# Performance work log

Measured on AMD Instinct MI355X. Metric: run time of the kernel, lower is better.

Reference implementation:

```python
import jax, jax.numpy as jnp
import numpy as np
from jax.scipy.special import logsumexp

UNK_ID = 1
B, T, V = 128, 33, 25000
E, H, D = 256, 256, 512
N, C = 8192, 16384
L = T - 1


def setup_inputs() -> dict:
    key = jax.random.key(0)
    ks = jax.random.split(key, 12)
    input_memories = jax.random.normal(ks[0], (N, D), jnp.float32)
    # each target owns a contiguous block of N//B memories (every segment non-empty)
    origin = jnp.repeat(jnp.arange(B, dtype=jnp.int32), N // B)
    initial_states = jax.random.normal(ks[1], (B, H), jnp.float32)
    target_token_ids = jax.random.randint(ks[2], (B, T), 0, V)
    # copyable elements: pick (memory n, time l); flat idx into [N,L] and [B,L]
    mem_pick = jax.random.randint(ks[3], (C,), 0, N)
    t_pick = jax.random.randint(ks[4], (C,), 0, L)
    copyable_elements_idxs = mem_pick * L + t_pick
    copyable_elements_sample_idxs = origin[mem_pick] * L + t_pick
    target_lengths = jax.random.randint(ks[5], (B,), 1, L + 1)
    emb_weight = 0.02 * jax.random.normal(ks[6], (V, E), jnp.float32)
    gru_w_ih = 0.05 * jax.random.normal(ks[7], (3 * H, E), jnp.float32)
    gru_w_hh = 0.05 * jax.random.normal(ks[8], (3 * H, H), jnp.float32)
    gru_b_ih = jnp.zeros((3 * H,), jnp.float32)
    gru_b_hh = jnp.zeros((3 * H,), jnp.float32)
    w_std_att = 0.05 * jax.random.normal(ks[9], (H, D), jnp.float32)
    w_copy_att = 0.05 * jax.random.normal(ks[10], (H, D), jnp.float32)
    hidden_to_vocab = 0.01 * jax.random.normal(ks[11], (2 * H, E), jnp.float32)
    vocab_bias = jnp.zeros((V,), jnp.float32)
    return dict(input_memories=input_memories, input_memories_origin_idx=origin,
                initial_states=initial_states, target_token_ids=target_token_ids,
                copyable_elements_idxs=copyable_elements_idxs,
                copyable_elements_sample_idxs=copyable_elements_sample_idxs,
                target_lengths=target_lengths, emb_weight=emb_weight,
                gru_w_ih=gru_w_ih, gru_w_hh=gru_w_hh, gru_b_ih=gru_b_ih,
                gru_b_hh=gru_b_hh, w_std_att=w_std_att, w_copy_att=w_copy_att,
                hidden_to_vocab=hidden_to_vocab, vocab_bias=vocab_bias)


def _gru(x, h0, w_ih, w_hh, b_ih, b_hh):
    # x: [B,L,E], h0: [B,H] -> outputs [B,L,H], last state [B,H]
    def step(h, xt):
        gi = xt @ w_ih.T + b_ih
        gh = h @ w_hh.T + b_hh
        ir, iz, inew = jnp.split(gi, 3, axis=-1)
        hr, hz, hnew = jnp.split(gh, 3, axis=-1)
        r = jax.nn.sigmoid(ir + hr)
        z = jax.nn.sigmoid(iz + hz)
        n = jnp.tanh(inew + r * hnew)
        h_next = (1.0 - z) * n + z * h
        return h_next, h_next
    h_last, ys = jax.lax.scan(step, h0, jnp.swapaxes(x, 0, 1))
    return jnp.swapaxes(ys, 0, 1), h_last


def _seg_log_softmax(x, idx, num_seg):
    m = jax.ops.segment_max(x, idx, num_segments=num_seg)
    x_sh = x - m[idx]
    s = jax.ops.segment_sum(jnp.exp(x_sh), idx, num_segments=num_seg)
    return x_sh - jnp.log(s)[idx]


def _seg_logsumexp(x, idx, num_seg):
    m = jax.ops.segment_max(x, idx, num_segments=num_seg)
    m_safe = jnp.where(jnp.isfinite(m), m, 0.0)
    s = jax.ops.segment_sum(jnp.exp(x - m_safe[idx]), idx, num_segments=num_seg)
    return jnp.where(s > 0, jnp.log(jnp.where(s > 0, s, 1.0)) + m_safe, -jnp.inf)


def reference(input_memories, input_memories_origin_idx, initial_states,
              target_token_ids, copyable_elements_idxs,
              copyable_elements_sample_idxs, target_lengths, emb_weight,
              gru_w_ih, gru_w_hh, gru_b_ih, gru_b_hh, w_std_att, w_copy_att,
              hidden_to_vocab, vocab_bias):
    origin = input_memories_origin_idx
    b, t = target_token_ids.shape
    l = t - 1
    tok_in = target_token_ids[:, :-1]
    tok_out = target_token_ids[:, 1:]

    x = emb_weight[tok_in]                                   # [B,L,E]
    out_states, _ = _gru(x, initial_states, gru_w_ih, gru_w_hh, gru_b_ih, gru_b_hh)
    std_reps = input_memories @ w_std_att.T                  # [N,H]
    copy_reps = input_memories @ w_copy_att.T                # [N,H]
    out_per_input = out_states[origin]                       # [N,L,H]
    std_scores = jnp.einsum('nlh,nh->nl', out_per_input, std_reps)
    copy_scores = jnp.einsum('nlh,nh->nl', out_per_input, copy_reps)

    std_logprobs = _seg_log_softmax(std_scores, origin, b)   # [N,L]
    std_mul = jnp.exp(std_logprobs)[:, :, None] * std_reps[:, None, :]
    std_out = jax.ops.segment_sum(std_mul, origin, num_segments=b)  # [B,L,H]

    cat = jnp.concatenate([std_out, out_states], axis=-1)    # [B,L,2H]
    target_scores = (cat @ hidden_to_vocab) @ emb_weight.T + vocab_bias  # [B,L,V]

    total_copy = _seg_logsumexp(copy_scores, origin, b)      # [B,L]
    all_scores = jnp.concatenate([target_scores, total_copy[:, :, None]], axis=-1)
    norm = logsumexp(all_scores, axis=-1)                    # [B,L]
    target_logprobs = target_scores - norm[:, :, None]
    copy_logprobs = copy_scores - norm[origin]               # [N,L]

    num_valid = jax.ops.segment_sum(jnp.ones_like(copyable_elements_sample_idxs),
                                    copyable_elements_sample_idxs,
                                    num_segments=b * l)
    valid_copy = num_valid.reshape(b, l) > 0
    unk_loc = tok_out == UNK_ID
    mask = valid_copy & unk_loc

    gen_lp = jnp.take_along_axis(target_logprobs, tok_out[:, :, None], axis=-1)[..., 0]
    gen_lp = jnp.where(mask, -jnp.inf, gen_lp)

    cc = _seg_logsumexp(copy_logprobs.reshape(-1)[copyable_elements_idxs],
                        copyable_elements_sample_idxs, b * l).reshape(b, l)

    any_lp = logsumexp(jnp.stack([gen_lp, cc]), axis=0)      # [B,L]
    len_mask = (jnp.arange(l)[None, :] < target_lengths[:, None]).astype(jnp.float32)
    per_seq = (any_lp * len_mask).sum(-1) / len_mask.sum(-1)
    return -per_seq.mean()
```

## Files before the change

kernel.cpp:

```cpp
#include <hip/hip_runtime.h>
#include <hip/hip_bf16.h>

#define UNK 1
constexpr int B  = 128, T = 33, V = 25000, E = 256, H = 256, D = 512;
constexpr int N  = 8192, C = 16384, L = 32;
constexpr int BL = B * L;
constexpr int VP = 25088;

typedef __attribute__((ext_vector_type(8))) short bf16x8;
typedef __attribute__((ext_vector_type(4))) float fx4;
typedef unsigned short u16;
typedef unsigned int u32;

__device__ __forceinline__ u16 f2b(float f) {
  u32 u = __float_as_uint(f);
  u += 0x7FFFu + ((u >> 16) & 1u);
  return (u16)(u >> 16);
}
__device__ __forceinline__ float b2f(u16 s) { return __uint_as_float(((u32)s) << 16); }
__device__ __forceinline__ float fsigm(float x) { return 1.f / (1.f + __expf(-x)); }
__device__ __forceinline__ float ftanh(float x) {
  float cx = fminf(fmaxf(x, -15.f), 15.f);
  float e = __expf(2.f * cx);
  return (e - 1.f) / (e + 1.f);
}
__device__ __forceinline__ u32 fkey(float f) {
  u32 b = __float_as_uint(f);
  return (b & 0x80000000u) ? ~b : (b | 0x80000000u);
}
__device__ __forceinline__ float fdec(u32 k) {
  u32 b = (k & 0x80000000u) ? (k & 0x7FFFFFFFu) : ~k;
  return __uint_as_float(b);
}
__device__ __forceinline__ void lcomb(float& M, float& S, float m2, float s2) {
  float Mn = fmaxf(M, m2);
  float a = (S  > 0.f) ? S  * expf(M  - Mn) : 0.f;
  float b = (s2 > 0.f) ? s2 * expf(m2 - Mn) : 0.f;
  M = Mn; S = a + b;
}
__device__ __forceinline__ void gload16(const void* g, void* l) {
  __builtin_amdgcn_global_load_lds(
      (const __attribute__((address_space(1))) void*)g,
      (__attribute__((address_space(3))) void*)l, 16, 0, 0);
}

__device__ __forceinline__ void cvt4_at(const float* in, u16* out, int i) {
  float4 v = *(const float4*)&in[i];
  u16 r[4] = { f2b(v.x), f2b(v.y), f2b(v.z), f2b(v.w) };
  *(ushort4*)&out[i] = *(ushort4*)r;
}

constexpr int EB_GI   = 192;
constexpr int P2_MEM  = N * D / 1024;
constexpr int P2_WHH  = 192;
constexpr int P2_WS   = 128;
constexpr int P2_WC   = 128;
constexpr int EB2_TOT = EB_GI + P2_MEM + P2_WHH + P2_WS + P2_WC;

__global__ __launch_bounds__(256, 2) void k_embgiB2(const int* __restrict__ tok,
    const float* __restrict__ emb, const float* __restrict__ wih,
    const float* __restrict__ bih, const float* __restrict__ bhh,
    float* __restrict__ Git,
    const float* __restrict__ mem, const float* __restrict__ whh,
    const float* __restrict__ wstd, const float* __restrict__ wcpy,
    u16* __restrict__ memb, u16* __restrict__ whb,
    u16* __restrict__ wsb, u16* __restrict__ wcb) {
  __shared__ __align__(16) u16 As[2][128 * 64];
  __shared__ __align__(16) u16 Bs2[2][128 * 64];
  int e = blockIdx.x, t = threadIdx.x;
  if (e >= EB_GI) {
    int b = e - EB_GI;
    if (b < P2_MEM) { cvt4_at(mem, memb, (b * 256 + t) * 4); return; }
    b -= P2_MEM;
    if (b < P2_WHH) { cvt4_at(whh, whb, (b * 256 + t) * 4); return; }
    b -= P2_WHH;
    if (b < P2_WS)  { cvt4_at(wstd, wsb, (b * 256 + t) * 4); return; }
    b -= P2_WS;
    cvt4_at(wcpy, wcb, (b * 256 + t) * 4);
    return;
  }
  int m0 = (e & 31) * 128, n0 = (e >> 5) * 128;
  int lane = t & 63, w = t >> 6, wm = w >> 1, wn = w & 1;
  int r16 = lane & 15, hi = lane >> 4;
  char* AsB = (char*)&As[0][0];
  char* BsB = (char*)&Bs2[0][0];
  int tk4[4];
#pragma unroll
  for (int i = 0; i < 4; ++i) {
    int row = (w * 4 + i) * 8 + (lane >> 3);
    int bl = m0 + row;
    tk4[i] = tok[(bl >> 5) * 33 + (bl & 31)];
  }
  fx4 acc[4][4] = {};
  auto stage = [&](int kt, int buf) {
#pragma unroll
    for (int i = 0; i < 4; ++i) {
      int row = (w * 4 + i) * 8 + (lane >> 3);
      int c = (lane & 7) ^ (row & 7);
      float4 a0 = *(const float4*)&emb[tk4[i] * 256 + kt * 64 + c * 8];
      float4 a1 = *(const float4*)&emb[tk4[i] * 256 + kt * 64 + c * 8 + 4];
      __align__(16) u16 ra[8] = { f2b(a0.x), f2b(a0.y), f2b(a0.z), f2b(a0.w),
                                  f2b(a1.x), f2b(a1.y), f2b(a1.z), f2b(a1.w) };
      *(int4*)(AsB + buf * 16384 + (w * 4 + i) * 1024 + lane * 16) = *(const int4*)ra;
      float4 b0 = *(const float4*)&wih[(n0 + row) * 256 + kt * 64 + c * 8];
      float4 b1 = *(const float4*)&wih[(n0 + row) * 256 + kt * 64 + c * 8 + 4];
      __align__(16) u16 rb[8] = { f2b(b0.x), f2b(b0.y), f2b(b0.z), f2b(b0.w),
                                  f2b(b1.x), f2b(b1.y), f2b(b1.z), f2b(b1.w) };
      *(int4*)(BsB + buf * 16384 + (w * 4 + i) * 1024 + lane * 16) = *(const int4*)rb;
    }
  };
  stage(0, 0);
  __syncthreads();
  for (int kt = 0; kt < 4; ++kt) {
    int buf = kt & 1;
    bf16x8 afr[4][2], bfr[4][2];
#pragma unroll
    for (int mi = 0; mi < 4; ++mi)
#pragma unroll
      for (int kk = 0; kk < 2; ++kk) {
        int row = wm * 64 + mi * 16 + r16, cc = kk * 4 + hi;
        afr[mi][kk] = *(const bf16x8*)(AsB + buf * 16384 + (row * 8 + (cc ^ (row & 7))) * 16);
      }
#pragma unroll
    for (int ni = 0; ni < 4; ++ni)
#pragma unroll
      for (int kk = 0; kk < 2; ++kk) {
        int row = wn * 64 + ni * 16 + r16, cc = kk * 4 + hi;
        bfr[ni][kk] = *(const bf16x8*)(BsB + buf * 16384 + (row * 8 + (cc ^ (row & 7))) * 16);
      }
    if (kt < 3) {
      stage(kt + 1, (kt + 1) & 1);
    }
#pragma unroll
    for (int kk = 0; kk < 2; ++kk)
#pragma unroll
      for (int mi = 0; mi < 4; ++mi)
#pragma unroll
        for (int ni = 0; ni < 4; ++ni)
          acc[mi][ni] = __builtin_amdgcn_mfma_f32_16x16x32_bf16(afr[mi][kk], bfr[ni][kk], acc[mi][ni], 0, 0, 0);
    __syncthreads();
  }
  float bihv[4];
#pragma unroll
  for (int ni = 0; ni < 4; ++ni) {
    int j = n0 + wn * 64 + ni * 16 + r16;
    bihv[ni] = bih[j] + (j < 512 ? bhh[j] : 0.f);
  }
#pragma unroll
  for (int mi = 0; mi < 4; ++mi)
#pragma unroll
    for (int ni = 0; ni < 4; ++ni)
#pragma unroll
      for (int q = 0; q < 4; ++q) {
        int bl = m0 + wm * 64 + mi * 16 + hi * 4 + q;
        int b = bl >> 5, st = bl & 31;
        int j  = n0 + wn * 64 + ni * 16 + r16;
        Git[(((size_t)(b >> 4) * 32 + st) * 768 + j) * 16 + (b & 15)] = acc[mi][ni][q] + bihv[ni];
      }
}

constexpr int GR_GRU  = 8;
constexpr int GR_REPS = 128;
constexpr int GR_EMB  = VP * E / 2048;
constexpr int GR_TR   = 256;
constexpr int GR_INIT = 8;
constexpr int GR_TOT  = GR_GRU + GR_REPS + GR_EMB + GR_TR + GR_INIT;

__global__ __launch_bounds__(512, 2) void k_grureps(
    const float* __restrict__ Git, const u16* __restrict__ whb,
    const float* __restrict__ bhh, const float* __restrict__ h0,
    u16* __restrict__ outsb,
    const u16* __restrict__ Am, const u16* __restrict__ wsb,
    const u16* __restrict__ wcb, float* __restrict__ sr, float* __restrict__ cr,
    const float* __restrict__ emb, const float* __restrict__ h2v,
    u16* __restrict__ embb, u16* __restrict__ h2vtb,
    u32* __restrict__ segk, float* __restrict__ segs,
    int* __restrict__ nval, float* __restrict__ lacc) {
  __shared__ __align__(16) char smem[147456];
  const int t = threadIdx.x;
  const int w = t >> 6, l = t & 63;

  if (blockIdx.x >= GR_GRU + GR_REPS) {
    int b = blockIdx.x - (GR_GRU + GR_REPS);
    if (b < GR_EMB) {
      int i = (b * 512 + t) * 4;
      if (i + 3 < V * E) cvt4_at(emb, embb, i);
      else for (int j = 0; j < 4; ++j) embb[i + j] = (i + j < V * E) ? f2b(emb[i + j]) : (u16)0;
      return;
    }
    b -= GR_EMB;
    if (b < GR_TR) {
      int f = b * 512 + t, j = f >> 9, k = f & 511;
      h2vtb[f] = f2b(h2v[k * 256 + j]);
      return;
    }
    b -= GR_TR;
    int i = b * 512 + t;
    if (i < BL) { segk[i] = 0x007FFFFFu; segs[i] = 0.f; nval[i] = 0; }
    if (i == 0) lacc[0] = 0.f;
    return;
  }

  if (blockIdx.x < GR_GRU) {
    u16* nfr = (u16*)smem;
    u16* hbf0 = (u16*)(smem + 131072);
    u16* hbf1 = (u16*)(smem + 131072 + 8192);
    const int lj = l & 15, lk = l >> 4;
    const int b0 = blockIdx.x * 16;

    bf16x8 fr[2][8], fz[2][8];
#pragma unroll
    for (int jh = 0; jh < 2; ++jh)
#pragma unroll
      for (int kc = 0; kc < 8; ++kc) {
        int jr = w * 32 + jh * 16 + lj;
        int k0 = kc * 32 + lk * 8;
        fr[jh][kc] = *(const bf16x8*)&whb[(0 * 256 + jr) * 256 + k0];
        fz[jh][kc] = *(const bf16x8*)&whb[(1 * 256 + jr) * 256 + k0];
        int4 nv = *(const int4*)&whb[(2 * 256 + jr) * 256 + k0];
        *(int4*)&nfr[((w * 16 + jh * 8 + kc) * 64 + l) * 8] = nv;
      }
    float bN[2];
#pragma unroll
    for (int jh = 0; jh < 2; ++jh) bN[jh] = bhh[512 + w * 32 + jh * 16 + lj];
    float hst[2][4];
#pragma unroll
    for (int jh = 0; jh < 2; ++jh)
#pragma unroll
      for (int q = 0; q < 4; ++q) {
        int m = lk * 4 + q, j = w * 32 + jh * 16 + lj;
        hst[jh][q] = h0[(b0 + m) * 256 + j];
        hbf0[m * 256 + (((j >> 3) ^ (m & 7)) * 8) + (j & 7)] = f2b(hst[jh][q]);
      }
    __syncthreads();

    for (int st = 0; st < 32; ++st) {
      const float* gb = Git + (size_t)(blockIdx.x * 32 + st) * 768 * 16;
      fx4 grz[4];
#pragma unroll
      for (int g = 0; g < 2; ++g)
#pragma unroll
        for (int jh = 0; jh < 2; ++jh)
          grz[g * 2 + jh] = *(const fx4*)&gb[(g * 256 + w * 32 + jh * 16 + lj) * 16 + lk * 4];
      fx4 gn[2];
      fx4 accR[2] = {}, accZ[2] = {}, accN[2] = {};
      const u16* hb = (st & 1) ? hbf1 : hbf0;
#pragma unroll
      for (int kc = 0; kc < 8; ++kc) {
        int k8 = kc * 4 + lk;
        bf16x8 a = *(const bf16x8*)&hb[lj * 256 + ((k8 ^ (lj & 7)) * 8)];
        bf16x8 nf0 = *(const bf16x8*)&nfr[((w * 16 + 0 + kc) * 64 + l) * 8];
        bf16x8 nf1 = *(const bf16x8*)&nfr[((w * 16 + 8 + kc) * 64 + l) * 8];
        accR[0] = __builtin_amdgcn_mfma_f32_16x16x32_bf16(a, fr[0][kc], accR[0], 0, 0, 0);
        accR[1] = __builtin_amdgcn_mfma_f32_16x16x32_bf16(a, fr[1][kc], accR[1], 0, 0, 0);
        accZ[0] = __builtin_amdgcn_mfma_f32_16x16x32_bf16(a, fz[0][kc], accZ[0], 0, 0, 0);
        accZ[1] = __builtin_amdgcn_mfma_f32_16x16x32_bf16(a, fz[1][kc], accZ[1], 0, 0, 0);
        accN[0] = __builtin_amdgcn_mfma_f32_16x16x32_bf16(a, nf0, accN[0], 0, 0, 0);
        accN[1] = __builtin_amdgcn_mfma_f32_16x16x32_bf16(a, nf1, accN[1], 0, 0, 0);
        if (kc == 5) {
#pragma unroll
          for (int jh = 0; jh < 2; ++jh)
            gn[jh] = *(const fx4*)&gb[(2 * 256 + w * 32 + jh * 16 + lj) * 16 + lk * 4];
        }
      }
      u16* hw = (st & 1) ? hbf0 : hbf1;
#pragma unroll
      for (int jh = 0; jh < 2; ++jh)
#pragma unroll
        for (int q = 0; q < 4; ++q) {
          float r = fsigm(grz[jh][q] + accR[jh][q]);
          float z = fsigm(grz[2 + jh][q] + accZ[jh][q]);
          float n = ftanh(gn[jh][q] + r * (accN[jh][q] + bN[jh]));
          float hn = (1.f - z) * n + z * hst[jh][q];
          hst[jh][q] = hn;
          int m = lk * 4 + q, j = w * 32 + jh * 16 + lj;
          u16 hbv = f2b(hn);
          hw[m * 256 + (((j >> 3) ^ (m & 7)) * 8) + (j & 7)] = hbv;
          outsb[((size_t)(b0 + m) * 32 + st) * 256 + j] = hbv;
        }
      __syncthreads();
    }
    return;
  }

  int rb = blockIdx.x - GR_GRU;
  int m0 = (rb >> 1) * 128, sn = rb & 1;
  const u16* Bsrc = sn ? wcb : wsb;
  int grp = w >> 2, wg = w & 3, wm = wg >> 1, wn = wg & 1;
  int jb = grp * 128;
  int lane = l, r16 = lane & 15, hi = lane >> 4;
  char* AsB = smem;
  char* BsB = smem + 32768 + grp * 32768;
  fx4 acc[4][4] = {};
  auto stage = [&](int kt, int buf) {
    if (grp == 0) {
#pragma unroll
      for (int i = 0; i < 4; ++i) {
        int s = (wg * 4 + i) * 64 + lane;
        int row = s >> 3, sw = s & 7, c = sw ^ (row & 7);
        gload16(&Am[(m0 + row) * 512 + kt * 64 + c * 8], AsB + buf * 16384 + (wg * 4 + i) * 1024);
        gload16(&Bsrc[(0 + row) * 512 + kt * 64 + c * 8], (smem + 32768) + buf * 16384 + (wg * 4 + i) * 1024);
      }
    } else {
#pragma unroll
      for (int i = 0; i < 4; ++i) {
        int s = (wg * 4 + i) * 64 + lane;
        int row = s >> 3, sw = s & 7, c = sw ^ (row & 7);
        gload16(&Bsrc[(128 + row) * 512 + kt * 64 + c * 8], (smem + 65536) + buf * 16384 + (wg * 4 + i) * 1024);
      }
    }
  };
  stage(0, 0);
  for (int kt = 0; kt < 8; ++kt) {
    __syncthreads();
    if (kt < 7) stage(kt + 1, (kt + 1) & 1);
    int buf = kt & 1;
    bf16x8 afr[4][2], bfr[4][2];
#pragma unroll
    for (int mi = 0; mi < 4; ++mi)
#pragma unroll
      for (int kk = 0; kk < 2; ++kk) {
        int row = wm * 64 + mi * 16 + r16, cc = kk * 4 + hi;
        afr[mi][kk] = *(const bf16x8*)(AsB + buf * 16384 + (row * 8 + (cc ^ (row & 7))) * 16);
      }
#pragma unroll
    for (int ni = 0; ni < 4; ++ni)
#pragma unroll
      for (int kk = 0; kk < 2; ++kk) {
        int row = wn * 64 + ni * 16 + r16, cc = kk * 4 + hi;
        bfr[ni][kk] = *(const bf16x8*)(BsB + buf * 16384 + (row * 8 + (cc ^ (row & 7))) * 16);
      }
#pragma unroll
    for (int kk = 0; kk < 2; ++kk)
#pragma unroll
      for (int mi = 0; mi < 4; ++mi)
#pragma unroll
        for (int ni = 0; ni < 4; ++ni)
          acc[mi][ni] = __builtin_amdgcn_mfma_f32_16x16x32_bf16(afr[mi][kk], bfr[ni][kk], acc[mi][ni], 0, 0, 0);
  }
#pragma unroll
  for (int mi = 0; mi < 4; ++mi)
#pragma unroll
    for (int ni = 0; ni < 4; ++ni)
#pragma unroll
      for (int q = 0; q < 4; ++q) {
        int mr = m0 + wm * 64 + mi * 16 + hi * 4 + q;
        int j  = sn * 256 + jb + wn * 64 + ni * 16 + r16;
        float vv = acc[mi][ni][q];
        if (j < 256) sr[mr * 256 + j] = vv; else cr[mr * 256 + (j - 256)] = vv;
      }
}

__global__ void k_scores(const u16* __restrict__ outsb, const float* __restrict__ sr,
                         const float* __restrict__ cr, float* __restrict__ ss,
                         float* __restrict__ cs) {
  __shared__ float os[32][257];
  int b = blockIdx.x >> 2, nc = blockIdx.x & 3, t = threadIdx.x;
  for (int i = 0; i < 8; ++i) {
    int q = t + 256 * i, row = q >> 6, c4 = q & 63;
    ushort4 v = *(const ushort4*)&outsb[(b * 32 + row) * 256 + c4 * 4];
    os[row][c4 * 4] = b2f(v.x); os[row][c4 * 4 + 1] = b2f(v.y);
    os[row][c4 * 4 + 2] = b2f(v.z); os[row][c4 * 4 + 3] = b2f(v.w);
  }
  __syncthreads();
  int l = t & 31, g = t >> 5;
  for (int rep = 0; rep < 2; ++rep) {
    int n = b * 64 + nc * 16 + g + rep * 8;
    float a = 0.f, c = 0.f;
    for (int k4 = 0; k4 < 64; ++k4) {
      float4 s4 = *(const float4*)&sr[n * 256 + k4 * 4];
      float4 c4v = *(const float4*)&cr[n * 256 + k4 * 4];
      float o0 = os[l][k4 * 4], o1 = os[l][k4 * 4 + 1];
      float o2 = os[l][k4 * 4 + 2], o3 = os[l][k4 * 4 + 3];
      a = fmaf(o0, s4.x, a); a = fmaf(o1, s4.y, a);
      a = fmaf(o2, s4.z, a); a = fmaf(o3, s4.w, a);
      c = fmaf(o0, c4v.x, c); c = fmaf(o1, c4v.y, c);
      c = fmaf(o2, c4v.z, c); c = fmaf(o3, c4v.w, c);
    }
    ss[n * 32 + l] = a; cs[n * 32 + l] = c;
  }
}

__global__ void k_smxseg(const float* __restrict__ ss, const float* __restrict__ cs,
                         const float* __restrict__ sr, u16* __restrict__ sob,
                         float* __restrict__ tc,
                         const int* __restrict__ idx, const int* __restrict__ sid,
                         u32* __restrict__ sk, int* __restrict__ nv) {
  __shared__ float wst[64][33];
  __shared__ float wcp[64][33];
  int e = blockIdx.x, t = threadIdx.x;
  if (e >= 128) {
    int c = (e - 128) * 256 + t;
    if (c < C) {
      int s = sid[c];
      atomicMax(&sk[s], fkey(cs[idx[c]]));
      atomicAdd(&nv[s], 1);
    }
    return;
  }
  int b = e;
  for (int i = 0; i < 8; ++i) {
    int q = t + 256 * i;
    wst[q >> 5][q & 31] = ss[b * 2048 + q];
    wcp[q >> 5][q & 31] = cs[b * 2048 + q];
  }
  __syncthreads();
  if (t < 32) {
    int l = t; float m = -1e30f;
    for (int n = 0; n < 64; ++n) m = fmaxf(m, wst[n][l]);
    float s = 0.f;
    for (int n = 0; n < 64; ++n) s += expf(wst[n][l] - m);
    float inv = 1.f / s;
    for (int n = 0; n < 64; ++n) wst[n][l] = expf(wst[n][l] - m) * inv;
  } else if (t < 64) {
    int l = t - 32; float m = -1e30f;
    for (int n = 0; n < 64; ++n) m = fmaxf(m, wcp[n][l]);
    float s = 0.f;
    for (int n = 0; n < 64; ++n) s += expf(wcp[n][l] - m);
    tc[b * 32 + l] = m + logf(s);
  }
  __syncthreads();
  float acc[32] = {};
  for (int n = 0; n < 64; ++n) {
    float v = sr[(b * 64 + n) * 256 + t];
#pragma unroll
    for (int l = 0; l < 32; ++l) acc[l] = fmaf(wst[n][l], v, acc[l]);
  }
  for (int l = 0; l < 32; ++l) sob[(b * 32 + l) * 256 + t] = f2b(acc[l]);
}

__global__ __launch_bounds__(256, 2) void k_projseg(const u16* __restrict__ sob,
    const u16* __restrict__ outsb, const u16* __restrict__ h2vtb,
    u16* __restrict__ pb,
    const int* __restrict__ idx, const int* __restrict__ sid,
    const float* __restrict__ cs, const u32* __restrict__ sk,
    float* __restrict__ ssum) {
  __shared__ __align__(16) u16 As[2][128 * 64];
  __shared__ __align__(16) u16 Bs2[2][128 * 64];
  int e = blockIdx.x, t = threadIdx.x;
  if (e >= 64) {
    int c = (e - 64) * 256 + t;
    if (c < C) {
      int s = sid[c];
      atomicAdd(&ssum[s], __expf(cs[idx[c]] - fdec(sk[s])));
    }
    return;
  }
  int m0 = (e & 31) * 128, n0 = (e >> 5) * 128;
  int lane = t & 63, w = t >> 6, wm = w >> 1, wn = w & 1;
  int r16 = lane & 15, hi = lane >> 4;
  char* AsB = (char*)&As[0][0];
  char* BsB = (char*)&Bs2[0][0];
  fx4 acc[4][4] = {};
  auto stage = [&](int kt, int buf) {
    const u16* Asrc = (kt < 4) ? sob : outsb;
    int ko = (kt & 3) * 64;
#pragma unroll
    for (int i = 0; i < 4; ++i) {
      int s = (w * 4 + i) * 64 + lane;
      int row = s >> 3, sw = s & 7, c = sw ^ (row & 7);
      gload16(&Asrc[(m0 + row) * 256 + ko + c * 8], AsB + buf * 16384 + (w * 4 + i) * 1024);
      gload16(&h2vtb[(n0 + row) * 512 + kt * 64 + c * 8], BsB + buf * 16384 + (w * 4 + i) * 1024);
    }
  };
  stage(0, 0);
  for (int kt = 0; kt < 8; ++kt) {
    __syncthreads();
    if (kt < 7) stage(kt + 1, (kt + 1) & 1);
    int buf = kt & 1;
    bf16x8 afr[4][2], bfr[4][2];
#pragma unroll
    for (int mi = 0; mi < 4; ++mi)
#pragma unroll
      for (int kk = 0; kk < 2; ++kk) {
        int row = wm * 64 + mi * 16 + r16, cc = kk * 4 + hi;
        afr[mi][kk] = *(const bf16x8*)(AsB + buf * 16384 + (row * 8 + (cc ^ (row & 7))) * 16);
      }
#pragma unroll
    for (int ni = 0; ni < 4; ++ni)
#pragma unroll
      for (int kk = 0; kk < 2; ++kk) {
        int row = wn * 64 + ni * 16 + r16, cc = kk * 4 + hi;
        bfr[ni][kk] = *(const bf16x8*)(BsB + buf * 16384 + (row * 8 + (cc ^ (row & 7))) * 16);
      }
#pragma unroll
    for (int kk = 0; kk < 2; ++kk)
#pragma unroll
      for (int mi = 0; mi < 4; ++mi)
#pragma unroll
        for (int ni = 0; ni < 4; ++ni)
          acc[mi][ni] = __builtin_amdgcn_mfma_f32_16x16x32_bf16(afr[mi][kk], bfr[ni][kk], acc[mi][ni], 0, 0, 0);
  }
#pragma unroll
  for (int mi = 0; mi < 4; ++mi)
#pragma unroll
    for (int ni = 0; ni < 4; ++ni)
#pragma unroll
      for (int q = 0; q < 4; ++q) {
        int mr = m0 + wm * 64 + mi * 16 + hi * 4 + q;
        int j  = n0 + wn * 64 + ni * 16 + r16;
        pb[mr * 256 + j] = f2b(acc[mi][ni][q]);
      }
}

__global__ __launch_bounds__(256, 2) void k_gemmgen(const u16* __restrict__ A,
    const u16* __restrict__ Bm, const float* __restrict__ vb,
    float* __restrict__ parts,
    const int* __restrict__ tok, float* __restrict__ gs) {
  __shared__ __align__(16) u16 Bs[2][64 * 256];
  __shared__ float red[2][128];
  int e = blockIdx.x, t = threadIdx.x;
  if (e >= 512) {
    int w = t >> 6, lane = t & 63;
    int row = (e - 512) * 4 + w;
    int b = row >> 5, l = row & 31;
    int tk = tok[b * 33 + l + 1];
    float s = 0.f;
#pragma unroll
    for (int i = 0; i < 4; ++i) {
      int k = lane * 4 + i;
      s += b2f(A[row * 256 + k]) * b2f(Bm[tk * 256 + k]);
    }
#pragma unroll
    for (int d = 1; d < 64; d <<= 1) s += __shfl_xor(s, d);
    if (lane == 0) gs[row] = s + vb[tk];
    return;
  }
  int vr = e & 15, mch = e >> 4;
  int m0 = mch * 128;
  int c0 = vr * 24 + min(vr, 8);
  int cn = 24 + (vr < 8 ? 1 : 0);
  int lane = t & 63, w = t >> 6, wm = w >> 1, wn = w & 1;
  int r16 = lane & 15, hi = lane >> 4;
  char* BsB = (char*)&Bs[0][0];
  const char* Bb = (const char*)Bm;

  bf16x8 af[4][8];
#pragma unroll
  for (int mi = 0; mi < 4; ++mi)
#pragma unroll
    for (int ks = 0; ks < 8; ++ks)
      af[mi][ks] = *(const bf16x8*)&A[(m0 + wm * 64 + mi * 16 + r16) * 256 + ks * 32 + hi * 8];

  int soff[8];
#pragma unroll
  for (int i = 0; i < 8; ++i) {
    int s = (w * 8 + i) * 64 + lane;
    int row = s >> 5, c = s & 31;
    int gc = (c & ~7) | ((c & 7) ^ (row & 7));
    soff[i] = row * 512 + gc * 16;
  }

  float Sa[4][4] = {};

#define STAGE(CG, BUF)                                                        \
  {                                                                           \
    _Pragma("unroll")                                                         \
    for (int i = 0; i < 8; ++i)                                               \
      gload16(Bb + (CG) * 32768 + soff[i],                                    \
              BsB + (BUF) * 32768 + w * 8192 + i * 1024);                     \
  }

  STAGE(c0, 0);
  for (int c = 0; c < cn; ++c) {
    int cg = c0 + c;
    __syncthreads();
    if (c + 1 < cn) STAGE(cg + 1, (c + 1) & 1);
    int buf = c & 1;
    fx4 acc[4][2] = {};
#pragma unroll
    for (int ks = 0; ks < 8; ++ks)
#pragma unroll
      for (int ni = 0; ni < 2; ++ni) {
        int row = wn * 32 + ni * 16 + r16;
        int g = ks * 4 + hi;
        int gp = (g & ~7) | ((g & 7) ^ (row & 7));
        bf16x8 bfv = *(const bf16x8*)(BsB + buf * 32768 + row * 512 + gp * 16);
#pragma unroll
        for (int mi = 0; mi < 4; ++mi)
          acc[mi][ni] = __builtin_amdgcn_mfma_f32_16x16x32_bf16(af[mi][ks], bfv, acc[mi][ni], 0, 0, 0);
      }
    float bias[2];
#pragma unroll
    for (int ni = 0; ni < 2; ++ni) {
      int v = cg * 64 + wn * 32 + ni * 16 + r16;
      bias[ni] = (v < V) ? vb[v] : -1e30f;
    }
#pragma unroll
    for (int mi = 0; mi < 4; ++mi)
#pragma unroll
      for (int q = 0; q < 4; ++q) {
        float ev = __expf(acc[mi][0][q] + bias[0]) + __expf(acc[mi][1][q] + bias[1]);
        Sa[mi][q] += ev;
      }
  }
#undef STAGE

#pragma unroll
  for (int mi = 0; mi < 4; ++mi)
#pragma unroll
    for (int q = 0; q < 4; ++q) {
      float s = Sa[mi][q];
#pragma unroll
      for (int d = 1; d < 16; d <<= 1) s += __shfl_xor(s, d);
      Sa[mi][q] = s;
    }
  if (r16 == 0) {
#pragma unroll
    for (int mi = 0; mi < 4; ++mi)
#pragma unroll
      for (int q = 0; q < 4; ++q)
        red[wn][wm * 64 + mi * 16 + hi * 4 + q] = Sa[mi][q];
  }
  __syncthreads();
  if (t < 128)
    parts[(size_t)(m0 + t) * 16 + vr] = red[0][t] + red[1][t];
}

__global__ void k_final(const float* __restrict__ parts, const float* __restrict__ tc,
                        const float* __restrict__ gs, const u32* __restrict__ sk,
                        const float* __restrict__ ssum, const int* __restrict__ nv,
                        const int* __restrict__ tok, const int* __restrict__ tlen,
                        float* __restrict__ lacc) {
  int i = blockIdx.x * 256 + threadIdx.x;
  int b = i >> 5, l = i & 31;
  float S = 0.f;
#pragma unroll
  for (int r = 0; r < 16; ++r) S += parts[(size_t)i * 16 + r];
  float M = 0.f, Ss = S;
  lcomb(M, Ss, tc[i], 1.f);
  float nrm = M + logf(Ss);
  int tk = tok[b * 33 + l + 1];
  float glp = gs[i] - nrm;
  int cnt = nv[i];
  if (cnt > 0 && tk == UNK) glp = -INFINITY;
  float cc = (cnt > 0) ? (logf(ssum[i]) + fdec(sk[i]) - nrm) : -INFINITY;
  float m = fmaxf(glp, cc);
  float any = (m == -INFINITY) ? -INFINITY : m + logf(expf(glp - m) + expf(cc - m));
  float oa = (l < tlen[b]) ? any : 0.f;
#pragma unroll
  for (int d = 1; d < 32; d <<= 1) oa += __shfl_xor(oa, d);
  if (l == 0) atomicAdd(lacc, oa / (float)tlen[b]);
}

__global__ void k_loss(const float* __restrict__ lacc, float* __restrict__ out) {
  out[0] = -lacc[0] / 128.f;
}

extern "C" void kernel_launch(void* const* d_in, const int* in_sizes, int n_in,
                              void* d_out, int out_size, void* d_ws, size_t ws_size,
                              hipStream_t stream) {
  const float* mem  = (const float*)d_in[0];
  const float* h0   = (const float*)d_in[2];
  const int*   tok  = (const int*)d_in[3];
  const int*   cidx = (const int*)d_in[4];
  const int*   csid = (const int*)d_in[5];
  const int*   tlen = (const int*)d_in[6];
  const float* emb  = (const float*)d_in[7];
  const float* wih  = (const float*)d_in[8];
  const float* whh  = (const float*)d_in[9];
  const float* bih  = (const float*)d_in[10];
  const float* bhh  = (const float*)d_in[11];
  const float* wstd = (const float*)d_in[12];
  const float* wcpy = (const float*)d_in[13];
  const float* h2v  = (const float*)d_in[14];
  const float* vb   = (const float*)d_in[15];

  char* ws = (char*)d_ws;
  size_t off = 0;
  auto alloc = [&](size_t bytes) -> char* {
    char* p = ws + off;
    off = (off + bytes + 255) & ~(size_t)255;
    return p;
  };
  u16*    embb  = (u16*)   alloc((size_t)VP * E * 2);
  u16*    memb  = (u16*)   alloc((size_t)N * D * 2);
  u16*    whb   = (u16*)   alloc(768 * 256 * 2);
  u16*    wsb   = (u16*)   alloc(256 * 512 * 2);
  u16*    wcb   = (u16*)   alloc(256 * 512 * 2);
  u16*    h2vtb = (u16*)   alloc(256 * 512 * 2);
  float*  Git   = (float*) alloc((size_t)BL * 768 * 4);
  u16*    outsb = (u16*)   alloc((size_t)BL * 256 * 2);
  u16*    stdob = (u16*)   alloc((size_t)BL * 256 * 2);
  float*  sreps = (float*) alloc((size_t)N * 256 * 4);
  float*  creps = (float*) alloc((size_t)N * 256 * 4);
  float*  sscr  = (float*) alloc((size_t)N * 32 * 4);
  float*  cscr  = (float*) alloc((size_t)N * 32 * 4);
  float*  tcopy = (float*) alloc(BL * 4);
  u16*    projb = (u16*)   alloc((size_t)BL * 256 * 2);
  float*  parts = (float*) alloc((size_t)BL * 16 * 4);
  float*  gens  = (float*) alloc(BL * 4);
  u32*    segk  = (u32*)   alloc(BL * 4);
  float*  segs  = (float*) alloc(BL * 4);
  int*    nval  = (int*)   alloc(BL * 4);
  float*  lacc  = (float*) alloc(256);
  (void)ws_size; (void)in_sizes; (void)n_in; (void)out_size;

  k_embgiB2<<<EB2_TOT, 256, 0, stream>>>(tok, emb, wih, bih, bhh, Git,
                                         mem, whh, wstd, wcpy,
                                         memb, whb, wsb, wcb);
  k_grureps<<<GR_TOT, 512, 0, stream>>>(Git, whb, bhh, h0, outsb,
                                        memb, wsb, wcb, sreps, creps,
                                        emb, h2v, embb, h2vtb,
                                        segk, segs, nval, lacc);
  k_scores<<<512, 256, 0, stream>>>(outsb, sreps, creps, sscr, cscr);
  k_smxseg<<<192, 256, 0, stream>>>(sscr, cscr, sreps, stdob, tcopy,
                                    cidx, csid, segk, nval);
  k_projseg<<<128, 256, 0, stream>>>(stdob, outsb, h2vtb, projb,
                                     cidx, csid, cscr, segk, segs);
  k_gemmgen<<<1536, 256, 0, stream>>>(projb, embb, vb, parts, tok, gens);
  k_final<<<16, 256, 0, stream>>>(parts, tcopy, gens, segk, segs, nval, tok, tlen, lacc);
  k_loss<<<1, 1, 0, stream>>>(lacc, (float*)d_out);
}
```

Before: 247.5 us.

## Fuse attention scores and softmax into one MFMA kernel with bf16 reps

Merges the scalar k_scores kernel and k_smxseg into one kernel per batch row. The kernel computes the std and copy scores with bf16 MFMA tiles, runs the softmax in shared memory and accumulates the weighted sum. The std/copy reps are now stored as bf16 instead of fp32, which halves their traffic, and the separate score round-trip through global memory is gone. The segment max/count and the exp-sum passes are each moved one kernel later (into k_projseg and extra k_gemmgen blocks) to keep their ordering. The price is lower precision in the reps and scores, and only 128 blocks for the fused kernel.

```diff
diff --git a/kernel.cpp b/kernel.cpp
--- a/kernel.cpp
+++ b/kernel.cpp
@@ -171,7 +171,7 @@
     const float* __restrict__ bhh, const float* __restrict__ h0,
     u16* __restrict__ outsb,
     const u16* __restrict__ Am, const u16* __restrict__ wsb,
-    const u16* __restrict__ wcb, float* __restrict__ sr, float* __restrict__ cr,
+    const u16* __restrict__ wcb, u16* __restrict__ srb, u16* __restrict__ crb,
     const float* __restrict__ emb, const float* __restrict__ h2v,
     u16* __restrict__ embb, u16* __restrict__ h2vtb,
     u32* __restrict__ segk, float* __restrict__ segs,
@@ -346,95 +346,120 @@
       for (int q = 0; q < 4; ++q) {
         int mr = m0 + wm * 64 + mi * 16 + hi * 4 + q;
         int j  = sn * 256 + jb + wn * 64 + ni * 16 + r16;
-        float vv = acc[mi][ni][q];
-        if (j < 256) sr[mr * 256 + j] = vv; else cr[mr * 256 + (j - 256)] = vv;
-      }
-}
-
-__global__ void k_scores(const u16* __restrict__ outsb, const float* __restrict__ sr,
-                         const float* __restrict__ cr, float* __restrict__ ss,
-                         float* __restrict__ cs) {
-  __shared__ float os[32][257];
-  int b = blockIdx.x >> 2, nc = blockIdx.x & 3, t = threadIdx.x;
-  for (int i = 0; i < 8; ++i) {
-    int q = t + 256 * i, row = q >> 6, c4 = q & 63;
-    ushort4 v = *(const ushort4*)&outsb[(b * 32 + row) * 256 + c4 * 4];
-    os[row][c4 * 4] = b2f(v.x); os[row][c4 * 4 + 1] = b2f(v.y);
-    os[row][c4 * 4 + 2] = b2f(v.z); os[row][c4 * 4 + 3] = b2f(v.w);
-  }
-  __syncthreads();
-  int l = t & 31, g = t >> 5;
-  for (int rep = 0; rep < 2; ++rep) {
-    int n = b * 64 + nc * 16 + g + rep * 8;
-    float a = 0.f, c = 0.f;
-    for (int k4 = 0; k4 < 64; ++k4) {
-      float4 s4 = *(const float4*)&sr[n * 256 + k4 * 4];
-      float4 c4v = *(const float4*)&cr[n * 256 + k4 * 4];
-      float o0 = os[l][k4 * 4], o1 = os[l][k4 * 4 + 1];
-      float o2 = os[l][k4 * 4 + 2], o3 = os[l][k4 * 4 + 3];
-      a = fmaf(o0, s4.x, a); a = fmaf(o1, s4.y, a);
-      a = fmaf(o2, s4.z, a); a = fmaf(o3, s4.w, a);
-      c = fmaf(o0, c4v.x, c); c = fmaf(o1, c4v.y, c);
-      c = fmaf(o2, c4v.z, c); c = fmaf(o3, c4v.w, c);
-    }
-    ss[n * 32 + l] = a; cs[n * 32 + l] = c;
-  }
-}
-
-__global__ void k_smxseg(const float* __restrict__ ss, const float* __restrict__ cs,
-                         const float* __restrict__ sr, u16* __restrict__ sob,
-                         float* __restrict__ tc,
-                         const int* __restrict__ idx, const int* __restrict__ sid,
-                         u32* __restrict__ sk, int* __restrict__ nv) {
+        u16 vv = f2b(acc[mi][ni][q]);
+        if (j < 256) srb[(size_t)mr * 256 + j] = vv;
+        else         crb[(size_t)mr * 256 + (j - 256)] = vv;
+      }
+}
+
+__global__ __launch_bounds__(256, 2) void k_scoresmx(
+    const u16* __restrict__ outsb, const u16* __restrict__ srb,
+    const u16* __restrict__ crb, u16* __restrict__ sob,
+    float* __restrict__ tc, float* __restrict__ cscr) {
+  __shared__ __align__(16) u16 As[2][32 * 64];
+  __shared__ __align__(16) u16 Bss[2][64 * 64];
+  __shared__ __align__(16) u16 Bcc[2][64 * 64];
   __shared__ float wst[64][33];
   __shared__ float wcp[64][33];
-  int e = blockIdx.x, t = threadIdx.x;
-  if (e >= 128) {
-    int c = (e - 128) * 256 + t;
-    if (c < C) {
-      int s = sid[c];
-      atomicMax(&sk[s], fkey(cs[idx[c]]));
-      atomicAdd(&nv[s], 1);
-    }
-    return;
-  }
-  int b = e;
+  int b = blockIdx.x, t = threadIdx.x;
+  int w = t >> 6, l = t & 63;
+  int r16 = l & 15, hi = l >> 4;
+  char* AsB = (char*)&As[0][0];
+  int typ = w >> 1, nh = w & 1;
+  const u16* Bp = typ ? crb : srb;
+  char* Bbase = typ ? (char*)&Bcc[0][0] : (char*)&Bss[0][0];
+
+  auto stage = [&](int kt, int buf) {
+    {
+      int row = w * 8 + (l >> 3);
+      int c = (l & 7) ^ (row & 7);
+      gload16(&outsb[(size_t)(b * 32 + row) * 256 + kt * 64 + c * 8],
+              AsB + buf * 4096 + w * 1024);
+    }
+#pragma unroll
+    for (int i = 0; i < 4; ++i) {
+      int s = (nh * 4 + i) * 64 + l;
+      int row = s >> 3, c = (s & 7) ^ (row & 7);
+      gload16(&Bp[(size_t)(b * 64 + row) * 256 + kt * 64 + c * 8],
+              Bbase + buf * 8192 + (nh * 4 + i) * 1024);
+    }
+  };
+  fx4 acc[2][2] = {};
+  stage(0, 0);
+  __syncthreads();
+  for (int kt = 0; kt < 4; ++kt) {
+    int buf = kt & 1;
+    bf16x8 af[2][2], bf[2][2];
+#pragma unroll
+    for (int mi = 0; mi < 2; ++mi)
+#pragma unroll
+      for (int kk = 0; kk < 2; ++kk) {
+        int row = mi * 16 + r16, cc = kk * 4 + hi;
+        af[mi][kk] = *(const bf16x8*)(AsB + buf * 4096 + (row * 8 + (cc ^ (row & 7))) * 16);
+      }
+#pragma unroll
+    for (int ni = 0; ni < 2; ++ni)
+#pragma unroll
+      for (int kk = 0; kk < 2; ++kk) {
+        int row = nh * 32 + ni * 16 + r16, cc = kk * 4 + hi;
+        bf[ni][kk] = *(const bf16x8*)(Bbase + buf * 8192 + (row * 8 + (cc ^ (row & 7))) * 16);
+      }
+    if (kt < 3) stage(kt + 1, (kt + 1) & 1);
+#pragma unroll
+    for (int kk = 0; kk < 2; ++kk)
+#pragma unroll
+      for (int mi = 0; mi < 2; ++mi)
+#pragma unroll
+        for (int ni = 0; ni < 2; ++ni)
+          acc[mi][ni] = __builtin_amdgcn_mfma_f32_16x16x32_bf16(af[mi][kk], bf[ni][kk], acc[mi][ni], 0, 0, 0);
+    __syncthreads();
+  }
+#pragma unroll
+  for (int mi = 0; mi < 2; ++mi)
+#pragma unroll
+    for (int ni = 0; ni < 2; ++ni)
+#pragma unroll
+      for (int q = 0; q < 4; ++q) {
+        int lr = mi * 16 + hi * 4 + q;
+        int nn = nh * 32 + ni * 16 + r16;
+        if (typ) wcp[nn][lr] = acc[mi][ni][q];
+        else     wst[nn][lr] = acc[mi][ni][q];
+      }
+  __syncthreads();
   for (int i = 0; i < 8; ++i) {
-    int q = t + 256 * i;
-    wst[q >> 5][q & 31] = ss[b * 2048 + q];
-    wcp[q >> 5][q & 31] = cs[b * 2048 + q];
+    int qd = t + 256 * i;
+    int nn = qd >> 5, lr = qd & 31;
+    cscr[(size_t)(b * 64 + nn) * 32 + lr] = wcp[nn][lr];
+  }
+  if (t < 32) {
+    int lr = t; float m = -1e30f;
+    for (int n = 0; n < 64; ++n) m = fmaxf(m, wst[n][lr]);
+    float s = 0.f;
+    for (int n = 0; n < 64; ++n) s += expf(wst[n][lr] - m);
+    float inv = 1.f / s;
+    for (int n = 0; n < 64; ++n) wst[n][lr] = expf(wst[n][lr] - m) * inv;
+  } else if (t < 64) {
+    int lr = t - 32; float m = -1e30f;
+    for (int n = 0; n < 64; ++n) m = fmaxf(m, wcp[n][lr]);
+    float s = 0.f;
+    for (int n = 0; n < 64; ++n) s += expf(wcp[n][lr] - m);
+    tc[b * 32 + lr] = m + logf(s);
   }
   __syncthreads();
-  if (t < 32) {
-    int l = t; float m = -1e30f;
-    for (int n = 0; n < 64; ++n) m = fmaxf(m, wst[n][l]);
-    float s = 0.f;
-    for (int n = 0; n < 64; ++n) s += expf(wst[n][l] - m);
-    float inv = 1.f / s;
-    for (int n = 0; n < 64; ++n) wst[n][l] = expf(wst[n][l] - m) * inv;
-  } else if (t < 64) {
-    int l = t - 32; float m = -1e30f;
-    for (int n = 0; n < 64; ++n) m = fmaxf(m, wcp[n][l]);
-    float s = 0.f;
-    for (int n = 0; n < 64; ++n) s += expf(wcp[n][l] - m);
-    tc[b * 32 + l] = m + logf(s);
-  }
-  __syncthreads();
-  float acc[32] = {};
+  float acc2[32] = {};
   for (int n = 0; n < 64; ++n) {
-    float v = sr[(b * 64 + n) * 256 + t];
-#pragma unroll
-    for (int l = 0; l < 32; ++l) acc[l] = fmaf(wst[n][l], v, acc[l]);
-  }
-  for (int l = 0; l < 32; ++l) sob[(b * 32 + l) * 256 + t] = f2b(acc[l]);
+    float v = b2f(srb[(size_t)(b * 64 + n) * 256 + t]);
+#pragma unroll
+    for (int lr = 0; lr < 32; ++lr) acc2[lr] = fmaf(wst[n][lr], v, acc2[lr]);
+  }
+  for (int lr = 0; lr < 32; ++lr) sob[(size_t)(b * 32 + lr) * 256 + t] = f2b(acc2[lr]);
 }
 
 __global__ __launch_bounds__(256, 2) void k_projseg(const u16* __restrict__ sob,
     const u16* __restrict__ outsb, const u16* __restrict__ h2vtb,
     u16* __restrict__ pb,
     const int* __restrict__ idx, const int* __restrict__ sid,
-    const float* __restrict__ cs, const u32* __restrict__ sk,
-    float* __restrict__ ssum) {
+    const float* __restrict__ cs, u32* __restrict__ sk, int* __restrict__ nv) {
   __shared__ __align__(16) u16 As[2][128 * 64];
   __shared__ __align__(16) u16 Bs2[2][128 * 64];
   int e = blockIdx.x, t = threadIdx.x;
@@ -442,7 +467,8 @@
     int c = (e - 64) * 256 + t;
     if (c < C) {
       int s = sid[c];
-      atomicAdd(&ssum[s], __expf(cs[idx[c]] - fdec(sk[s])));
+      atomicMax(&sk[s], fkey(cs[idx[c]]));
+      atomicAdd(&nv[s], 1);
     }
     return;
   }
@@ -506,10 +532,21 @@
 __global__ __launch_bounds__(256, 2) void k_gemmgen(const u16* __restrict__ A,
     const u16* __restrict__ Bm, const float* __restrict__ vb,
     float* __restrict__ parts,
-    const int* __restrict__ tok, float* __restrict__ gs) {
+    const int* __restrict__ tok, float* __restrict__ gs,
+    const int* __restrict__ idx, const int* __restrict__ sid,
+    const float* __restrict__ cs, const u32* __restrict__ sk,
+    float* __restrict__ ssum) {
   __shared__ __align__(16) u16 Bs[2][64 * 256];
   __shared__ float red[2][128];
   int e = blockIdx.x, t = threadIdx.x;
+  if (e >= 1536) {
+    int c = (e - 1536) * 256 + t;
+    if (c < C) {
+      int s = sid[c];
+      atomicAdd(&ssum[s], __expf(cs[idx[c]] - fdec(sk[s])));
+    }
+    return;
+  }
   if (e >= 512) {
     int w = t >> 6, lane = t & 63;
     int row = (e - 512) * 4 + w;
@@ -682,9 +719,8 @@
   float*  Git   = (float*) alloc((size_t)BL * 768 * 4);
   u16*    outsb = (u16*)   alloc((size_t)BL * 256 * 2);
   u16*    stdob = (u16*)   alloc((size_t)BL * 256 * 2);
-  float*  sreps = (float*) alloc((size_t)N * 256 * 4);
-  float*  creps = (float*) alloc((size_t)N * 256 * 4);
-  float*  sscr  = (float*) alloc((size_t)N * 32 * 4);
+  u16*    srb   = (u16*)   alloc((size_t)N * 256 * 2);
+  u16*    crb   = (u16*)   alloc((size_t)N * 256 * 2);
   float*  cscr  = (float*) alloc((size_t)N * 32 * 4);
   float*  tcopy = (float*) alloc(BL * 4);
   u16*    projb = (u16*)   alloc((size_t)BL * 256 * 2);
@@ -700,15 +736,14 @@
                                          mem, whh, wstd, wcpy,
                                          memb, whb, wsb, wcb);
   k_grureps<<<GR_TOT, 512, 0, stream>>>(Git, whb, bhh, h0, outsb,
-                                        memb, wsb, wcb, sreps, creps,
+                                        memb, wsb, wcb, srb, crb,
                                         emb, h2v, embb, h2vtb,
                                         segk, segs, nval, lacc);
-  k_scores<<<512, 256, 0, stream>>>(outsb, sreps, creps, sscr, cscr);
-  k_smxseg<<<192, 256, 0, stream>>>(sscr, cscr, sreps, stdob, tcopy,
-                                    cidx, csid, segk, nval);
+  k_scoresmx<<<128, 256, 0, stream>>>(outsb, srb, crb, stdob, tcopy, cscr);
   k_projseg<<<128, 256, 0, stream>>>(stdob, outsb, h2vtb, projb,
-                                     cidx, csid, cscr, segk, segs);
-  k_gemmgen<<<1536, 256, 0, stream>>>(projb, embb, vb, parts, tok, gens);
+                                     cidx, csid, cscr, segk, nval);
+  k_gemmgen<<<1600, 256, 0, stream>>>(projb, embb, vb, parts, tok, gens,
+                                      cidx, csid, cscr, segk, segs);
   k_final<<<16, 256, 0, stream>>>(parts, tcopy, gens, segk, segs, nval, tok, tlen, lacc);
   k_loss<<<1, 1, 0, stream>>>(lacc, (float*)d_out);
 }
```

After: 231.0 us. 6.7% less time.
